# Kernel optimization log

Measured on AMD Instinct MI355X. Metric: run time of the kernel, lower is better.

Reference implementation:

```python
import jax, jax.numpy as jnp
import numpy as np


def setup_inputs() -> dict:
    key = jax.random.key(0)
    ks = jax.random.split(key, 7)
    B, D, d1, d2, d3 = 256, 256, 1024, 512, 256
    s = lambda f: 1.0 / np.sqrt(f)  # torch nn.Linear-style init scale
    return {
        "x": jax.random.normal(ks[0], (B, D), jnp.float32),
        "W1": jax.random.normal(ks[1], (d1, D), jnp.float32) * s(D),
        "b1": jax.random.normal(ks[2], (d1,), jnp.float32) * s(D),
        "W2": jax.random.normal(ks[3], (d2, d1), jnp.float32) * s(d1),
        "b2": jax.random.normal(ks[4], (d2,), jnp.float32) * s(d1),
        "W3": jax.random.normal(ks[5], (d3, d2), jnp.float32) * s(d2),
        "b3": jax.random.normal(ks[6], (d3,), jnp.float32) * s(d2),
        "k": 10,
    }


def _border_dists(x, W1, b1, W2, b2, W3, b3):
    # Layer 1: pre-activations and boundary distances. For the first layer the
    # effective linear map is W1 itself (shared across the batch).
    z1 = x @ W1.T + b1                                   # [B, d1]
    dist1 = jnp.abs(z1) / jnp.linalg.norm(W1, axis=1)    # [B, d1]
    m1 = (z1 > 0).astype(x.dtype)
    V1 = m1[:, :, None] * W1[None]                       # [B, d1, D] per-instance map after ReLU
    h1 = m1 * z1

    # Layer 2
    z2 = h1 @ W2.T + b2                                  # [B, d2]
    V2 = jnp.einsum('oi,bid->bod', W2, V1)               # [B, d2, D]
    dist2 = jnp.abs(z2) / jnp.linalg.norm(V2, axis=2)
    m2 = (z2 > 0).astype(x.dtype)
    h2 = m2 * z2

    # Layer 3
    z3 = h2 @ W3.T + b3                                  # [B, d3]
    V3 = jnp.einsum('oi,bid->bod', W3, m2[:, :, None] * V2)  # [B, d3, D]
    dist3 = jnp.abs(z3) / jnp.linalg.norm(V3, axis=2)

    return jnp.concatenate([dist1, dist2, dist3], axis=1)  # [B, d1+d2+d3]


def reference(x, W1, b1, W2, b2, W3, b3, k):
    dists = _border_dists(x, W1, b1, W2, b2, W3, b3)
    # smallest-k distances per instance via top_k on negated distances
    neg_top, _ = jax.lax.top_k(-dists, k)                # [B, k]
    return jnp.sum(-neg_top)                             # border-distance loss (scalar)
```

## Files before the change

kernel.cpp:

```cpp
#include <hip/hip_runtime.h>
#include <math.h>
#include <float.h>

#define B   256
#define D   256
#define D1  1024
#define D2  512
#define D3  256
#define NDIST (D1 + D2 + D3)
#define CQ  2.0f

typedef __attribute__((ext_vector_type(8))) short short8;
typedef __attribute__((ext_vector_type(4))) float f32x4;
typedef __attribute__((ext_vector_type(4))) int   i32x4;

__device__ __forceinline__ float waveReduceSum(float v) {
    #pragma unroll
    for (int off = 32; off > 0; off >>= 1)
        v += __shfl_down(v, off, 64);
    return v;
}
__device__ __forceinline__ float waveReduceMax(float v) {
    #pragma unroll
    for (int off = 32; off > 0; off >>= 1)
        v = fmaxf(v, __shfl_down(v, off, 64));
    return v;
}
__device__ __forceinline__ unsigned short f2bf(float f) {
    unsigned int u = __float_as_uint(f);
    u = (u + 0x7FFFu + ((u >> 16) & 1u)) >> 16;
    return (unsigned short)u;
}
__device__ __forceinline__ float bf2f(unsigned short h) {
    return __uint_as_float(((unsigned int)h) << 16);
}
__device__ __forceinline__ void gld16(const void* g, void* l) {
    __builtin_amdgcn_global_load_lds(
        (const __attribute__((address_space(1))) unsigned int*)g,
        (__attribute__((address_space(3))) unsigned int*)l, 16, 0, 0);
}
__device__ __forceinline__ int swz_src(int row, int lane) {
    return ((lane & 3) + ((row >> 1) & 3)) & 3;
}
__device__ __forceinline__ int swz_frag(int row, int quad) {
    return row * 32 + (((quad - ((row >> 1) & 3)) & 3) * 8);
}

__device__ __forceinline__ void split_job(const float* src, unsigned short* hi,
                                          unsigned short* lo, int off) {
    float4 v = *(const float4*)(src + off);
    ushort4 h, l;
    h.x = f2bf(v.x); l.x = f2bf(v.x - bf2f(h.x));
    h.y = f2bf(v.y); l.y = f2bf(v.y - bf2f(h.y));
    h.z = f2bf(v.z); l.z = f2bf(v.z - bf2f(h.z));
    h.w = f2bf(v.w); l.w = f2bf(v.w - bf2f(h.w));
    *(ushort4*)(hi + off) = h;
    *(ushort4*)(lo + off) = l;
}

__device__ __forceinline__ void split8(const float* p, short8& h8, short8& l8) {
    float4 a = *(const float4*)(p);
    float4 b = *(const float4*)(p + 4);
    float hv[8] = { a.x, a.y, a.z, a.w, b.x, b.y, b.z, b.w };
    #pragma unroll
    for (int q = 0; q < 8; q++) {
        unsigned short hh = f2bf(hv[q]);
        h8[q] = (short)hh;
        l8[q] = (short)f2bf(hv[q] - bf2f(hh));
    }
}

template <int KD, int KL>
__device__ __forceinline__ void mfma3_64(
    const unsigned short* __restrict__ Ahi, const unsigned short* __restrict__ Alo,
    const unsigned short* __restrict__ Bhi, const unsigned short* __restrict__ Blo,
    int m0, int n0, int k0, unsigned short* sm, f32x4 acc[2][2]) {
    int tid = threadIdx.x;
    int l = tid & 63, w = tid >> 6;
    int rsub = l >> 2;
    int quad = l >> 4, l16 = l & 15;
    int wm = (w >> 1) * 32, wn = (w & 1) * 32;
    unsigned short* sAh = sm;
    unsigned short* sAl = sm + 2048;
    unsigned short* sBh = sm + 4096;
    unsigned short* sBl = sm + 6144;
    ptrdiff_t dA = Alo - Ahi, dB = Blo - Bhi;
    int rloc = w * 16 + rsub;
    int c = swz_src(rloc, l);
    const unsigned short* pa = Ahi + (size_t)(m0 + rloc) * KD + k0 + c * 8;
    const unsigned short* pb = Bhi + (size_t)(n0 + rloc) * KD + k0 + c * 8;
    int aoff[2], boff[2];
    #pragma unroll
    for (int mt = 0; mt < 2; mt++) aoff[mt] = swz_frag(wm + mt * 16 + l16, quad);
    #pragma unroll
    for (int nt = 0; nt < 2; nt++) boff[nt] = swz_frag(wn + nt * 16 + l16, quad);
    for (int kk = 0; kk < KL; kk += 32) {
        gld16(pa + kk,      sAh + w * 512);
        gld16(pa + dA + kk, sAl + w * 512);
        gld16(pb + kk,      sBh + w * 512);
        gld16(pb + dB + kk, sBl + w * 512);
        __syncthreads();
        short8 ah[2], al[2], bh[2], bl[2];
        #pragma unroll
        for (int mt = 0; mt < 2; mt++) {
            ah[mt] = *(const short8*)(sAh + aoff[mt]);
            al[mt] = *(const short8*)(sAl + aoff[mt]);
        }
        #pragma unroll
        for (int nt = 0; nt < 2; nt++) {
            bh[nt] = *(const short8*)(sBh + boff[nt]);
            bl[nt] = *(const short8*)(sBl + boff[nt]);
        }
        #pragma unroll
        for (int mt = 0; mt < 2; mt++)
            #pragma unroll
            for (int nt = 0; nt < 2; nt++) {
                acc[mt][nt] = __builtin_amdgcn_mfma_f32_16x16x32_bf16(ah[mt], bh[nt], acc[mt][nt], 0, 0, 0);
                acc[mt][nt] = __builtin_amdgcn_mfma_f32_16x16x32_bf16(ah[mt], bl[nt], acc[mt][nt], 0, 0, 0);
                acc[mt][nt] = __builtin_amdgcn_mfma_f32_16x16x32_bf16(al[mt], bh[nt], acc[mt][nt], 0, 0, 0);
            }
        __syncthreads();
    }
}

__global__ __launch_bounds__(256) void k_l1p(
    const float* __restrict__ x, const float* __restrict__ W1,
    const float* __restrict__ W2, const float* __restrict__ W3,
    const float* __restrict__ b1,
    float* __restrict__ dists, unsigned char* __restrict__ m1q,
    unsigned short* __restrict__ h1hi, unsigned short* __restrict__ h1lo,
    float* __restrict__ zeros, float* __restrict__ outp,
    unsigned short* __restrict__ W2hi, unsigned short* __restrict__ W2lo,
    unsigned short* __restrict__ W3hi, unsigned short* __restrict__ W3lo,
    signed char* __restrict__ W1Ti8, float* __restrict__ saq,
    signed char* __restrict__ W2i8,  float* __restrict__ sbq,
    signed char* __restrict__ W3i8,  float* __restrict__ s3q,
    float* __restrict__ rn1) {
    __shared__ __align__(16) unsigned short sm[8192];
    int blk = blockIdx.x;
    int t = threadIdx.x;

    if (blk < 64) {
        unsigned short* sAh = sm;
        unsigned short* sAl = sm + 2048;
        unsigned short* sBh = sm + 4096;
        unsigned short* sBl = sm + 6144;
        int m0 = (blk & 3) * 64, n0 = (blk >> 2) * 64;
        int l = t & 63, w = t >> 6;
        int rsub = l >> 2;
        int quad = l >> 4, l16 = l & 15;
        int wm = (w >> 1) * 32, wn = (w & 1) * 32;
        int rloc = w * 16 + rsub;
        int c = swz_src(rloc, l);
        const float* pax = x + (size_t)(m0 + rloc) * D + c * 8;
        const float* pbw = W1 + (size_t)(n0 + rloc) * D + c * 8;
        int aoff[2], boff[2];
        #pragma unroll
        for (int mt = 0; mt < 2; mt++) aoff[mt] = swz_frag(wm + mt * 16 + l16, quad);
        #pragma unroll
        for (int nt = 0; nt < 2; nt++) boff[nt] = swz_frag(wn + nt * 16 + l16, quad);
        int wrA = w * 512 + l * 8;
        f32x4 acc[2][2] = {};
        for (int kk = 0; kk < D; kk += 32) {
            short8 ha, la, hb, lb;
            split8(pax + kk, ha, la);
            split8(pbw + kk, hb, lb);
            *(short8*)(sAh + wrA) = ha;
            *(short8*)(sAl + wrA) = la;
            *(short8*)(sBh + wrA) = hb;
            *(short8*)(sBl + wrA) = lb;
            __syncthreads();
            short8 ah[2], al[2], bh[2], bl[2];
            #pragma unroll
            for (int mt = 0; mt < 2; mt++) {
                ah[mt] = *(const short8*)(sAh + aoff[mt]);
                al[mt] = *(const short8*)(sAl + aoff[mt]);
            }
            #pragma unroll
            for (int nt = 0; nt < 2; nt++) {
                bh[nt] = *(const short8*)(sBh + boff[nt]);
                bl[nt] = *(const short8*)(sBl + boff[nt]);
            }
            #pragma unroll
            for (int mt = 0; mt < 2; mt++)
                #pragma unroll
                for (int nt = 0; nt < 2; nt++) {
                    acc[mt][nt] = __builtin_amdgcn_mfma_f32_16x16x32_bf16(ah[mt], bh[nt], acc[mt][nt], 0, 0, 0);
                    acc[mt][nt] = __builtin_amdgcn_mfma_f32_16x16x32_bf16(ah[mt], bl[nt], acc[mt][nt], 0, 0, 0);
                    acc[mt][nt] = __builtin_amdgcn_mfma_f32_16x16x32_bf16(al[mt], bh[nt], acc[mt][nt], 0, 0, 0);
                }
            __syncthreads();
        }
        #pragma unroll
        for (int mt = 0; mt < 2; mt++)
            #pragma unroll
            for (int nt = 0; nt < 2; nt++) {
                int n = n0 + wn + nt * 16 + l16;
                float bv = b1[n];
                #pragma unroll
                for (int r = 0; r < 4; r++) {
                    int m = m0 + wm + mt * 16 + quad * 4 + r;
                    float z = acc[mt][nt][r] + bv;
                    size_t idx = (size_t)m * D1 + n;
                    dists[idx] = fabsf(z);
                    m1q[idx] = (z > 0.f) ? 0xFFu : 0u;
                    float h = z > 0.f ? z : 0.f;
                    unsigned short hh = f2bf(h);
                    h1hi[idx] = hh;
                    h1lo[idx] = f2bf(h - bf2f(hh));
                }
            }
        return;
    }
    if (blk < 448) {
        if (blk == 64 && t == 0) outp[0] = 0.f;
        int i4 = (blk - 64) * 1024 + t * 4;
        *(float4*)(zeros + i4) = make_float4(0.f, 0.f, 0.f, 0.f);
        return;
    }
    if (blk < 960) {
        split_job(W2, W2hi, W2lo, (blk - 448) * 1024 + t * 4);
        return;
    }
    if (blk < 1088) {
        split_job(W3, W3hi, W3lo, (blk - 960) * 1024 + t * 4);
        return;
    }
    if (blk < 1120) {
        int ty = t >> 5, tx = t & 31;
        int d = (blk - 1088) * 8 + ty;
        float m = 0.f;
        for (int i = tx; i < D1; i += 32) m = fmaxf(m, fabsf(W1[(size_t)i * D + d]));
        #pragma unroll
        for (int off = 16; off > 0; off >>= 1) m = fmaxf(m, __shfl_down(m, off, 32));
        m = __shfl(m, 0, 32);
        m = fmaxf(m, 1e-20f);
        if (tx == 0) saq[d] = m / 127.f;
        float inv = 127.f / m;
        for (int i = tx; i < D1; i += 32) {
            int q = __float2int_rn(W1[(size_t)i * D + d] * inv);
            W1Ti8[(size_t)d * D1 + i] = (signed char)q;
        }
        return;
    }
    if (blk < 1248) {
        int o = (blk - 1120) * 4 + (t >> 6);
        int l = t & 63;
        const float* row = W2 + (size_t)o * D1;
        float m = 0.f;
        for (int tt = l; tt < D1; tt += 64) m = fmaxf(m, fabsf(row[tt]));
        m = waveReduceMax(m);
        m = __shfl(m, 0, 64);
        m = fmaxf(m, 1e-20f);
        if (l == 0) sbq[o] = m / 127.f;
        float inv = 127.f / m;
        for (int tt = l; tt < D1; tt += 64)
            W2i8[(size_t)o * D1 + tt] = (signed char)__float2int_rn(row[tt] * inv);
        return;
    }
    if (blk < 1312) {
        int p = (blk - 1248) * 4 + (t >> 6);
        int l = t & 63;
        const float* row = W3 + (size_t)p * D2;
        float m = 0.f;
        for (int tt = l; tt < D2; tt += 64) m = fmaxf(m, fabsf(row[tt]));
        m = waveReduceMax(m);
        m = __shfl(m, 0, 64);
        m = fmaxf(m, 1e-20f);
        if (l == 0) s3q[p] = m / 127.f;
        float inv = 127.f / m;
        for (int tt = l; tt < D2; tt += 64)
            W3i8[(size_t)p * D2 + tt] = (signed char)__float2int_rn(row[tt] * inv);
        return;
    }
    {
        int gw = (blk - 1312) * 4 + (t >> 6);
        int lane = t & 63;
        const float* row = W1 + (size_t)gw * D;
        float s = 0.f;
        for (int tt = lane; tt < D; tt += 64) { float v = row[tt]; s += v * v; }
        s = waveReduceSum(s);
        if (lane == 0) rn1[gw] = sqrtf(s);
    }
}

__global__ __launch_bounds__(256) void k_big1(
    const unsigned short* __restrict__ h1hi, const unsigned short* __restrict__ h1lo,
    const unsigned short* __restrict__ W2hi, const unsigned short* __restrict__ W2lo,
    float* __restrict__ z2,
    const signed char* __restrict__ W1Ti8,
    const signed char* __restrict__ W2i8,
    const unsigned char* __restrict__ m1q,
    const float* __restrict__ saq,
    const float* __restrict__ sbq,
    signed char* __restrict__ qV2,
    float* __restrict__ norm2) {
    __shared__ __align__(16) unsigned char smem[65536];
    int bid = blockIdx.x;

    if (bid < 128) {
        unsigned short* sm = (unsigned short*)smem;
        int m0 = (bid & 3) * 64, n0 = ((bid >> 2) & 7) * 64, k0 = (bid >> 5) * 256;
        f32x4 acc[2][2] = {};
        mfma3_64<D1, 256>(h1hi, h1lo, W2hi, W2lo, m0, n0, k0, sm, acc);
        int l = threadIdx.x & 63, w = threadIdx.x >> 6;
        int quad = l >> 4, l16 = l & 15;
        int wm = (w >> 1) * 32, wn = (w & 1) * 32;
        #pragma unroll
        for (int mt = 0; mt < 2; mt++)
            #pragma unroll
            for (int nt = 0; nt < 2; nt++) {
                int n = n0 + wn + nt * 16 + l16;
                #pragma unroll
                for (int r = 0; r < 4; r++) {
                    int m = m0 + wm + mt * 16 + quad * 4 + r;
                    atomicAdd(&z2[(size_t)m * D2 + n], acc[mt][nt][r]);
                }
            }
        return;
    }

    int j = bid - 128;
    int m0 = (j & 1) * 128;
    int o0 = ((j >> 1) & 3) * 128;
    int b = j >> 3;
    int tid = threadIdx.x;
    int l = tid & 63, w = tid >> 6;
    int quad = l >> 4, l16 = l & 15;
    int wm = (w >> 1) * 64, wn = (w & 1) * 64;
    const unsigned char* mrow = m1q + (size_t)b * D1;

    const signed char* pa[4];
    const signed char* pb[4];
    int lrow = l >> 3, ls = l & 7;
    #pragma unroll
    for (int r = 0; r < 4; r++) {
        int row = r * 32 + w * 8 + lrow;
        int c = (ls + (row & 7)) & 7;
        pa[r] = W1Ti8 + (size_t)(m0 + row) * D1 + c * 16;
        pb[r] = W2i8 + (size_t)(o0 + row) * D1 + c * 16;
    }
    int aoff[4][2], boff[4][2];
    #pragma unroll
    for (int mt = 0; mt < 4; mt++) {
        int tr = wm + mt * 16 + l16;
        #pragma unroll
        for (int ks = 0; ks < 2; ks++)
            aoff[mt][ks] = tr * 128 + (((ks * 4 + quad) - (tr & 7)) & 7) * 16;
    }
    #pragma unroll
    for (int nt = 0; nt < 4; nt++) {
        int tr = wn + nt * 16 + l16;
        #pragma unroll
        for (int ks = 0; ks < 2; ks++)
            boff[nt][ks] = tr * 128 + (((ks * 4 + quad) - (tr & 7)) & 7) * 16;
    }

    i32x4 acc[4][4];
    #pragma unroll
    for (int i = 0; i < 4; i++)
        #pragma unroll
        for (int jj = 0; jj < 4; jj++) acc[i][jj] = (i32x4)0;

    {
        signed char* buf0 = (signed char*)smem;
        #pragma unroll
        for (int r = 0; r < 4; r++) {
            gld16(pa[r], buf0 + r * 4096 + w * 1024);
            gld16(pb[r], buf0 + 16384 + r * 4096 + w * 1024);
        }
    }
    i32x4 mv0 = *(const i32x4*)(mrow + quad * 16);
    i32x4 mv1 = *(const i32x4*)(mrow + 64 + quad * 16);
    __syncthreads();

    #pragma unroll
    for (int t = 0; t < 8; t++) {
        signed char* bufc = (signed char*)smem + ((t & 1) << 15);
        signed char* bufn = (signed char*)smem + (((t + 1) & 1) << 15);
        i32x4 nmv0 = mv0, nmv1 = mv1;
        if (t < 7) {
            int kn = (t + 1) * 128;
            #pragma unroll
            for (int r = 0; r < 4; r++) {
                gld16(pa[r] + kn, bufn + r * 4096 + w * 1024);
                gld16(pb[r] + kn, bufn + 16384 + r * 4096 + w * 1024);
            }
            nmv0 = *(const i32x4*)(mrow + kn + quad * 16);
            nmv1 = *(const i32x4*)(mrow + kn + 64 + quad * 16);
        }
        const signed char* As = bufc;
        const signed char* Bs = bufc + 16384;
        #pragma unroll
        for (int ks = 0; ks < 2; ks++) {
            i32x4 mv = ks ? mv1 : mv0;
            i32x4 a[4], bq[4];
            #pragma unroll
            for (int mt = 0; mt < 4; mt++)
                a[mt] = (*(const i32x4*)(As + aoff[mt][ks])) & mv;
            #pragma unroll
            for (int nt = 0; nt < 4; nt++)
                bq[nt] = *(const i32x4*)(Bs + boff[nt][ks]);
            #pragma unroll
            for (int mt = 0; mt < 4; mt++)
                #pragma unroll
                for (int nt = 0; nt < 4; nt++)
                    acc[mt][nt] = __builtin_amdgcn_mfma_i32_16x16x64_i8(
                        a[mt], bq[nt], acc[mt][nt], 0, 0, 0);
        }
        __syncthreads();
        mv0 = nmv0; mv1 = nmv1;
    }

    float sad[4][4];
    #pragma unroll
    for (int mt = 0; mt < 4; mt++)
        #pragma unroll
        for (int r = 0; r < 4; r++)
            sad[mt][r] = saq[m0 + wm + mt * 16 + quad * 4 + r];
    float sbv[4], sbdq[4];
    #pragma unroll
    for (int nt = 0; nt < 4; nt++) {
        sbv[nt] = sbq[o0 + wn + nt * 16 + l16];
        sbdq[nt] = sbv[nt] * (1.0f / CQ);
    }

    float nrm[4] = {0.f, 0.f, 0.f, 0.f};
    signed char* qb = qV2 + (size_t)b * (D * D2);
    #pragma unroll
    for (int mt = 0; mt < 4; mt++) {
        int dbase = m0 + wm + mt * 16 + quad * 4;
        #pragma unroll
        for (int r = 0; r < 4; r++) {
            float sa = sad[mt][r];
            size_t rowoff = (size_t)(dbase + r) * D2;
            #pragma unroll
            for (int nt = 0; nt < 4; nt++) {
                float tv = (float)acc[mt][nt][r];
                float u = tv * sa;
                nrm[nt] = fmaf(u, u, nrm[nt]);
                int qi = __float2int_rn(tv * sbdq[nt]);
                qi = max(-127, min(127, qi));
                qb[rowoff + o0 + wn + nt * 16 + l16] = (signed char)qi;
            }
        }
    }
    #pragma unroll
    for (int nt = 0; nt < 4; nt++) {
        float s = nrm[nt] * (sbv[nt] * sbv[nt]);
        s += __shfl_down(s, 32, 64);
        s += __shfl_down(s, 16, 64);
        if (l < 16)
            atomicAdd(&norm2[(size_t)b * D2 + o0 + wn + nt * 16 + l], s);
    }
}

__global__ __launch_bounds__(256) void k_big2(
    const float* __restrict__ z2,
    const float* __restrict__ b2,
    const unsigned short* __restrict__ W3hi, const unsigned short* __restrict__ W3lo,
    float* __restrict__ z3,
    const signed char* __restrict__ W3i8,
    const signed char* __restrict__ qV2,
    const float* __restrict__ saq,
    const float* __restrict__ s3q,
    float* __restrict__ norm3) {
    __shared__ __align__(16) unsigned char smem[66048];
    int bid = blockIdx.x;
    int tid = threadIdx.x;

    if (bid < 32) {
        unsigned short* sAh = (unsigned short*)smem;
        unsigned short* sAl = sAh + 2048;
        unsigned short* sBh = sAh + 4096;
        unsigned short* sBl = sAh + 6144;
        int m0 = (bid & 3) * 64, n0 = ((bid >> 2) & 3) * 64, k0 = (bid >> 4) * 256;
        int l = tid & 63, w = tid >> 6;
        int rsub = l >> 2;
        int quad = l >> 4, l16 = l & 15;
        int wm = (w >> 1) * 32, wn = (w & 1) * 32;
        int rloc = w * 16 + rsub;
        int c = swz_src(rloc, l);
        const float* pz  = z2 + (size_t)(m0 + rloc) * D2 + k0 + c * 8;
        const float* pbi = b2 + k0 + c * 8;
        const unsigned short* pb = W3hi + (size_t)(n0 + rloc) * D2 + k0 + c * 8;
        ptrdiff_t dB = W3lo - W3hi;
        int aoff[2], boff[2];
        #pragma unroll
        for (int mt = 0; mt < 2; mt++) aoff[mt] = swz_frag(wm + mt * 16 + l16, quad);
        #pragma unroll
        for (int nt = 0; nt < 2; nt++) boff[nt] = swz_frag(wn + nt * 16 + l16, quad);
        int wrA = w * 512 + l * 8;
        f32x4 acc[2][2] = {};
        for (int kk = 0; kk < 256; kk += 32) {
            gld16(pb + kk,      sBh + w * 512);
            gld16(pb + dB + kk, sBl + w * 512);
            float4 za = *(const float4*)(pz + kk);
            float4 zb = *(const float4*)(pz + kk + 4);
            float4 ba = *(const float4*)(pbi + kk);
            float4 bb = *(const float4*)(pbi + kk + 4);
            float hv[8] = { za.x + ba.x, za.y + ba.y, za.z + ba.z, za.w + ba.w,
                            zb.x + bb.x, zb.y + bb.y, zb.z + bb.z, zb.w + bb.w };
            short8 h8, l8;
            #pragma unroll
            for (int q2 = 0; q2 < 8; q2++) {
                float h = hv[q2] > 0.f ? hv[q2] : 0.f;
                unsigned short hh = f2bf(h);
                h8[q2] = (short)hh;
                l8[q2] = (short)f2bf(h - bf2f(hh));
            }
            *(short8*)(sAh + wrA) = h8;
            *(short8*)(sAl + wrA) = l8;
            __syncthreads();
            short8 ah[2], al[2], bh[2], bl[2];
            #pragma unroll
            for (int mt = 0; mt < 2; mt++) {
                ah[mt] = *(const short8*)(sAh + aoff[mt]);
                al[mt] = *(const short8*)(sAl + aoff[mt]);
            }
            #pragma unroll
            for (int nt = 0; nt < 2; nt++) {
                bh[nt] = *(const short8*)(sBh + boff[nt]);
                bl[nt] = *(const short8*)(sBl + boff[nt]);
            }
            #pragma unroll
            for (int mt = 0; mt < 2; mt++)
                #pragma unroll
                for (int nt = 0; nt < 2; nt++) {
                    acc[mt][nt] = __builtin_amdgcn_mfma_f32_16x16x32_bf16(ah[mt], bh[nt], acc[mt][nt], 0, 0, 0);
                    acc[mt][nt] = __builtin_amdgcn_mfma_f32_16x16x32_bf16(ah[mt], bl[nt], acc[mt][nt], 0, 0, 0);
                    acc[mt][nt] = __builtin_amdgcn_mfma_f32_16x16x32_bf16(al[mt], bh[nt], acc[mt][nt], 0, 0, 0);
                }
            __syncthreads();
        }
        #pragma unroll
        for (int mt = 0; mt < 2; mt++)
            #pragma unroll
            for (int nt = 0; nt < 2; nt++) {
                int n = n0 + wn + nt * 16 + l16;
                #pragma unroll
                for (int r = 0; r < 4; r++) {
                    int m = m0 + wm + mt * 16 + quad * 4 + r;
                    atomicAdd(&z3[(size_t)m * D3 + n], acc[mt][nt][r]);
                }
            }
        return;
    }

    int j = bid - 32;
    unsigned char* mbuf = (unsigned char*)smem + 65536;
    int m0 = (j & 1) * 128;
    int n0 = ((j >> 1) & 1) * 128;
    int bc = j >> 2;
    int l = tid & 63, w = tid >> 6;
    int quad = l >> 4, l16 = l & 15;
    int wm = (w >> 1) * 64, wn = (w & 1) * 64;
    const signed char* Bsrc = qV2 + (size_t)bc * (D * D2);

    {
        #pragma unroll
        for (int rr = 0; rr < 2; rr++) {
            int o = tid * 2 + rr;
            float z = z2[(size_t)bc * D2 + o] + b2[o];
            mbuf[o] = (z > 0.f) ? 0xFFu : 0u;
        }
    }

    const signed char* pa[4];
    const signed char* pb[4];
    int lrow = l >> 3, ls = l & 7;
    #pragma unroll
    for (int r = 0; r < 4; r++) {
        int row = r * 32 + w * 8 + lrow;
        int c = (ls + (row & 7)) & 7;
        pa[r] = W3i8 + (size_t)(m0 + row) * D2 + c * 16;
        pb[r] = Bsrc + (size_t)(n0 + row) * D2 + c * 16;
    }
    int aoff[4][2], boff[4][2];
    #pragma unroll
    for (int mt = 0; mt < 4; mt++) {
        int tr = wm + mt * 16 + l16;
        #pragma unroll
        for (int ks = 0; ks < 2; ks++)
            aoff[mt][ks] = tr * 128 + (((ks * 4 + quad) - (tr & 7)) & 7) * 16;
    }
    #pragma unroll
    for (int nt = 0; nt < 4; nt++) {
        int tr = wn + nt * 16 + l16;
        #pragma unroll
        for (int ks = 0; ks < 2; ks++)
            boff[nt][ks] = tr * 128 + (((ks * 4 + quad) - (tr & 7)) & 7) * 16;
    }

    i32x4 acc[4][4];
    #pragma unroll
    for (int i = 0; i < 4; i++)
        #pragma unroll
        for (int jj = 0; jj < 4; jj++) acc[i][jj] = (i32x4)0;

    {
        signed char* buf0 = (signed char*)smem;
        #pragma unroll
        for (int r = 0; r < 4; r++) {
            gld16(pa[r], buf0 + r * 4096 + w * 1024);
            gld16(pb[r], buf0 + 16384 + r * 4096 + w * 1024);
        }
    }
    __syncthreads();

    #pragma unroll
    for (int t = 0; t < 4; t++) {
        signed char* bufc = (signed char*)smem + ((t & 1) << 15);
        signed char* bufn = (signed char*)smem + (((t + 1) & 1) << 15);
        if (t < 3) {
            int kn = (t + 1) * 128;
            #pragma unroll
            for (int r = 0; r < 4; r++) {
                gld16(pa[r] + kn, bufn + r * 4096 + w * 1024);
                gld16(pb[r] + kn, bufn + 16384 + r * 4096 + w * 1024);
            }
        }
        int kk = t * 128;
        i32x4 mv0 = *(const i32x4*)(mbuf + kk + quad * 16);
        i32x4 mv1 = *(const i32x4*)(mbuf + kk + 64 + quad * 16);
        const signed char* As = bufc;
        const signed char* Bs = bufc + 16384;
        #pragma unroll
        for (int ks = 0; ks < 2; ks++) {
            i32x4 mv = ks ? mv1 : mv0;
            i32x4 a[4], bq[4];
            #pragma unroll
            for (int mt = 0; mt < 4; mt++)
                a[mt] = *(const i32x4*)(As + aoff[mt][ks]);
            #pragma unroll
            for (int nt = 0; nt < 4; nt++)
                bq[nt] = (*(const i32x4*)(Bs + boff[nt][ks])) & mv;
            #pragma unroll
            for (int mt = 0; mt < 4; mt++)
                #pragma unroll
                for (int nt = 0; nt < 4; nt++)
                    acc[mt][nt] = __builtin_amdgcn_mfma_i32_16x16x64_i8(
                        a[mt], bq[nt], acc[mt][nt], 0, 0, 0);
        }
        __syncthreads();
    }

    float saCQ[4];
    #pragma unroll
    for (int nt = 0; nt < 4; nt++)
        saCQ[nt] = saq[n0 + wn + nt * 16 + l16] * CQ;

    #pragma unroll
    for (int mt = 0; mt < 4; mt++)
        #pragma unroll
        for (int r = 0; r < 4; r++) {
            float s = 0.f;
            #pragma unroll
            for (int nt = 0; nt < 4; nt++) {
                float v = (float)acc[mt][nt][r] * saCQ[nt];
                s += v * v;
            }
            s += __shfl_down(s, 8, 64);
            s += __shfl_down(s, 4, 64);
            s += __shfl_down(s, 2, 64);
            s += __shfl_down(s, 1, 64);
            if (l16 == 0) {
                int p = m0 + wm + mt * 16 + quad * 4 + r;
                float s3 = s3q[p];
                atomicAdd(&norm3[(size_t)bc * D3 + p], s * s3 * s3);
            }
        }
}

__global__ __launch_bounds__(256) void k_topk(
    const float* __restrict__ dists,
    const float* __restrict__ rn1,
    const float* __restrict__ z2, const float* __restrict__ b2,
    const float* __restrict__ norm2,
    const float* __restrict__ z3, const float* __restrict__ b3,
    const float* __restrict__ norm3,
    const int* __restrict__ kp, float* __restrict__ outp) {
    int t = threadIdx.x;
    int wv = t >> 6, lane = t & 63;
    int b = blockIdx.x * 4 + wv;
    float lv[28];
    #pragma unroll
    for (int j = 0; j < 16; j++) {
        int n = lane + 64 * j;
        lv[j] = dists[(size_t)b * D1 + n] / rn1[n];
    }
    #pragma unroll
    for (int j = 16; j < 24; j++) {
        int o = lane + 64 * (j - 16);
        float zz = z2[(size_t)b * D2 + o] + b2[o];
        lv[j] = fabsf(zz) / sqrtf(norm2[(size_t)b * D2 + o]);
    }
    #pragma unroll
    for (int j = 24; j < 28; j++) {
        int p = lane + 64 * (j - 24);
        float zz = z3[(size_t)b * D3 + p] + b3[p];
        lv[j] = fabsf(zz) / sqrtf(norm3[(size_t)b * D3 + p]);
    }
    int k = *kp;
    if (k > NDIST) k = NDIST;
    float sum = 0.f;
    for (int it = 0; it < k; it++) {
        float mv = lv[0]; int mj = 0;
        #pragma unroll
        for (int j = 1; j < 28; j++)
            if (lv[j] < mv) { mv = lv[j]; mj = j; }
        unsigned long long key =
            ((unsigned long long)__float_as_uint(mv) << 32) | (unsigned)(lane * 32 + mj);
        #pragma unroll
        for (int off = 1; off < 64; off <<= 1) {
            unsigned long long o = __shfl_xor(key, off, 64);
            if (o < key) key = o;
        }
        sum += __uint_as_float((unsigned)(key >> 32));
        int wl = (int)((key >> 5) & 63u), wj = (int)(key & 31u);
        if (lane == wl) lv[wj] = FLT_MAX;
    }
    if (lane == 0) atomicAdd(outp, sum);
}

extern "C" void kernel_launch(void* const* d_in, const int* in_sizes, int n_in,
                              void* d_out, int out_size, void* d_ws, size_t ws_size,
                              hipStream_t stream) {
    const float* x  = (const float*)d_in[0];
    const float* W1 = (const float*)d_in[1];
    const float* b1 = (const float*)d_in[2];
    const float* W2 = (const float*)d_in[3];
    const float* b2 = (const float*)d_in[4];
    const float* W3 = (const float*)d_in[5];
    const float* b3 = (const float*)d_in[6];
    const int*   kp = (const int*)d_in[7];
    float* outp = (float*)d_out;

    float* fp = (float*)d_ws;
    float* rn1     = fp;                          fp += D1;
    float* dists   = fp;                          fp += (size_t)B * D1;
    float* saq     = fp;                          fp += D;
    float* sbq     = fp;                          fp += D2;
    float* s3q     = fp;                          fp += D3;
    float* z2      = fp;                          fp += (size_t)B * D2;
    float* z3      = fp;                          fp += (size_t)B * D3;
    float* norm2   = fp;                          fp += (size_t)B * D2;
    float* norm3   = fp;                          fp += (size_t)B * D3;
    unsigned short* up = (unsigned short*)fp;
    unsigned short* W2hi  = up;  up += (size_t)D2 * D1;
    unsigned short* W2lo  = up;  up += (size_t)D2 * D1;
    unsigned short* W3hi  = up;  up += (size_t)D3 * D2;
    unsigned short* W3lo  = up;  up += (size_t)D3 * D2;
    unsigned short* h1hi  = up;  up += (size_t)B * D1;
    unsigned short* h1lo  = up;  up += (size_t)B * D1;
    signed char*    cp = (signed char*)up;
    signed char*    W1Ti8 = cp;  cp += (size_t)D * D1;
    signed char*    W2i8  = cp;  cp += (size_t)D2 * D1;
    signed char*    W3i8  = cp;  cp += (size_t)D3 * D2;
    unsigned char*  m1q   = (unsigned char*)cp;  cp += (size_t)B * D1;
    signed char*    qV2   = cp;

    k_l1p<<<1568, 256, 0, stream>>>(x, W1, W2, W3, b1,
                                    dists, m1q, h1hi, h1lo,
                                    z2, outp, W2hi, W2lo, W3hi, W3lo,
                                    W1Ti8, saq, W2i8, sbq, W3i8, s3q, rn1);

    k_big1<<<2176, 256, 0, stream>>>(h1hi, h1lo, W2hi, W2lo, z2,
                                     W1Ti8, W2i8, m1q, saq, sbq, qV2, norm2);

    k_big2<<<1056, 256, 0, stream>>>(z2, b2, W3hi, W3lo, z3,
                                     W3i8, qV2, saq, s3q, norm3);

    k_topk<<<B / 4, 256, 0, stream>>>(dists, rn1, z2, b2, norm2, z3, b3, norm3,
                                      kp, outp);
}
```

Baseline: 175.4 us.

## Process two batch rows per k_big1 block and single-buffer k_big2 tiles

k_big1 now computes two batch instances per block, reusing each loaded W1T/W2 tile for two sets of masked MFMAs. That halves the global loads of the weight tiles and the block count, at the cost of double the accumulator registers. Launch bounds now request 2 blocks per CU, and the mask rows are staged in shared memory. k_big2 drops its double buffering in favour of a single 32KB tile buffer so more blocks fit per CU, which gives up load/compute overlap inside a block.

Result: faster. 160.9 us (-8.3%).

```diff
diff --git a/kernel.cpp b/kernel.cpp
--- a/kernel.cpp
+++ b/kernel.cpp
@@ -284,7 +284,7 @@
     }
 }
 
-__global__ __launch_bounds__(256) void k_big1(
+__global__ __launch_bounds__(256, 2) void k_big1(
     const unsigned short* __restrict__ h1hi, const unsigned short* __restrict__ h1lo,
     const unsigned short* __restrict__ W2hi, const unsigned short* __restrict__ W2lo,
     float* __restrict__ z2,
@@ -295,7 +295,7 @@
     const float* __restrict__ sbq,
     signed char* __restrict__ qV2,
     float* __restrict__ norm2) {
-    __shared__ __align__(16) unsigned char smem[65536];
+    __shared__ __align__(16) unsigned char smem[67584];
     int bid = blockIdx.x;
 
     if (bid < 128) {
@@ -323,12 +323,14 @@
     int j = bid - 128;
     int m0 = (j & 1) * 128;
     int o0 = ((j >> 1) & 3) * 128;
-    int b = j >> 3;
+    int b0 = (j >> 3) * 2;
     int tid = threadIdx.x;
     int l = tid & 63, w = tid >> 6;
     int quad = l >> 4, l16 = l & 15;
     int wm = (w >> 1) * 64, wn = (w & 1) * 64;
-    const unsigned char* mrow = m1q + (size_t)b * D1;
+    unsigned char* mbuf = (unsigned char*)smem + 65536;
+
+    *(int2*)(mbuf + tid * 8) = *(const int2*)(m1q + (size_t)b0 * D1 + tid * 8);
 
     const signed char* pa[4];
     const signed char* pb[4];
@@ -356,11 +358,13 @@
             boff[nt][ks] = tr * 128 + (((ks * 4 + quad) - (tr & 7)) & 7) * 16;
     }
 
-    i32x4 acc[4][4];
-    #pragma unroll
-    for (int i = 0; i < 4; i++)
-        #pragma unroll
-        for (int jj = 0; jj < 4; jj++) acc[i][jj] = (i32x4)0;
+    i32x4 acc[2][4][4];
+    #pragma unroll
+    for (int g = 0; g < 2; g++)
+        #pragma unroll
+        for (int i = 0; i < 4; i++)
+            #pragma unroll
+            for (int jj = 0; jj < 4; jj++) acc[g][i][jj] = (i32x4)0;
 
     {
         signed char* buf0 = (signed char*)smem;
@@ -370,15 +374,12 @@
             gld16(pb[r], buf0 + 16384 + r * 4096 + w * 1024);
         }
     }
-    i32x4 mv0 = *(const i32x4*)(mrow + quad * 16);
-    i32x4 mv1 = *(const i32x4*)(mrow + 64 + quad * 16);
     __syncthreads();
 
     #pragma unroll
     for (int t = 0; t < 8; t++) {
         signed char* bufc = (signed char*)smem + ((t & 1) << 15);
         signed char* bufn = (signed char*)smem + (((t + 1) & 1) << 15);
-        i32x4 nmv0 = mv0, nmv1 = mv1;
         if (t < 7) {
             int kn = (t + 1) * 128;
             #pragma unroll
@@ -386,30 +387,35 @@
                 gld16(pa[r] + kn, bufn + r * 4096 + w * 1024);
                 gld16(pb[r] + kn, bufn + 16384 + r * 4096 + w * 1024);
             }
-            nmv0 = *(const i32x4*)(mrow + kn + quad * 16);
-            nmv1 = *(const i32x4*)(mrow + kn + 64 + quad * 16);
         }
         const signed char* As = bufc;
         const signed char* Bs = bufc + 16384;
         #pragma unroll
         for (int ks = 0; ks < 2; ks++) {
-            i32x4 mv = ks ? mv1 : mv0;
+            i32x4 mva = *(const i32x4*)(mbuf +        t * 128 + ks * 64 + quad * 16);
+            i32x4 mvb = *(const i32x4*)(mbuf + 1024 + t * 128 + ks * 64 + quad * 16);
             i32x4 a[4], bq[4];
             #pragma unroll
             for (int mt = 0; mt < 4; mt++)
-                a[mt] = (*(const i32x4*)(As + aoff[mt][ks])) & mv;
+                a[mt] = *(const i32x4*)(As + aoff[mt][ks]);
             #pragma unroll
             for (int nt = 0; nt < 4; nt++)
                 bq[nt] = *(const i32x4*)(Bs + boff[nt][ks]);
             #pragma unroll
-            for (int mt = 0; mt < 4; mt++)
+            for (int mt = 0; mt < 4; mt++) {
+                i32x4 a0 = a[mt] & mva;
+                i32x4 a1 = a[mt] & mvb;
                 #pragma unroll
                 for (int nt = 0; nt < 4; nt++)
-                    acc[mt][nt] = __builtin_amdgcn_mfma_i32_16x16x64_i8(
-                        a[mt], bq[nt], acc[mt][nt], 0, 0, 0);
+                    acc[0][mt][nt] = __builtin_amdgcn_mfma_i32_16x16x64_i8(
+                        a0, bq[nt], acc[0][mt][nt], 0, 0, 0);
+                #pragma unroll
+                for (int nt = 0; nt < 4; nt++)
+                    acc[1][mt][nt] = __builtin_amdgcn_mfma_i32_16x16x64_i8(
+                        a1, bq[nt], acc[1][mt][nt], 0, 0, 0);
+            }
         }
         __syncthreads();
-        mv0 = nmv0; mv1 = nmv1;
     }
 
     float sad[4][4];
@@ -425,33 +431,37 @@
         sbdq[nt] = sbv[nt] * (1.0f / CQ);
     }
 
-    float nrm[4] = {0.f, 0.f, 0.f, 0.f};
-    signed char* qb = qV2 + (size_t)b * (D * D2);
-    #pragma unroll
-    for (int mt = 0; mt < 4; mt++) {
-        int dbase = m0 + wm + mt * 16 + quad * 4;
-        #pragma unroll
-        for (int r = 0; r < 4; r++) {
-            float sa = sad[mt][r];
-            size_t rowoff = (size_t)(dbase + r) * D2;
-            #pragma unroll
-            for (int nt = 0; nt < 4; nt++) {
-                float tv = (float)acc[mt][nt][r];
-                float u = tv * sa;
-                nrm[nt] = fmaf(u, u, nrm[nt]);
-                int qi = __float2int_rn(tv * sbdq[nt]);
-                qi = max(-127, min(127, qi));
-                qb[rowoff + o0 + wn + nt * 16 + l16] = (signed char)qi;
-            }
-        }
-    }
-    #pragma unroll
-    for (int nt = 0; nt < 4; nt++) {
-        float s = nrm[nt] * (sbv[nt] * sbv[nt]);
-        s += __shfl_down(s, 32, 64);
-        s += __shfl_down(s, 16, 64);
-        if (l < 16)
-            atomicAdd(&norm2[(size_t)b * D2 + o0 + wn + nt * 16 + l], s);
+    #pragma unroll
+    for (int g = 0; g < 2; g++) {
+        int bg = b0 + g;
+        float nrm[4] = {0.f, 0.f, 0.f, 0.f};
+        signed char* qb = qV2 + (size_t)bg * (D * D2);
+        #pragma unroll
+        for (int mt = 0; mt < 4; mt++) {
+            int dbase = m0 + wm + mt * 16 + quad * 4;
+            #pragma unroll
+            for (int r = 0; r < 4; r++) {
+                float sa = sad[mt][r];
+                size_t rowoff = (size_t)(dbase + r) * D2;
+                #pragma unroll
+                for (int nt = 0; nt < 4; nt++) {
+                    float tv = (float)acc[g][mt][nt][r];
+                    float u = tv * sa;
+                    nrm[nt] = fmaf(u, u, nrm[nt]);
+                    int qi = __float2int_rn(tv * sbdq[nt]);
+                    qi = max(-127, min(127, qi));
+                    qb[rowoff + o0 + wn + nt * 16 + l16] = (signed char)qi;
+                }
+            }
+        }
+        #pragma unroll
+        for (int nt = 0; nt < 4; nt++) {
+            float s = nrm[nt] * (sbv[nt] * sbv[nt]);
+            s += __shfl_down(s, 32, 64);
+            s += __shfl_down(s, 16, 64);
+            if (l < 16)
+                atomicAdd(&norm2[(size_t)bg * D2 + o0 + wn + nt * 16 + l], s);
+        }
     }
 }
 
@@ -465,7 +475,7 @@
     const float* __restrict__ saq,
     const float* __restrict__ s3q,
     float* __restrict__ norm3) {
-    __shared__ __align__(16) unsigned char smem[66048];
+    __shared__ __align__(16) unsigned char smem[33280];
     int bid = blockIdx.x;
     int tid = threadIdx.x;
 
@@ -548,7 +558,9 @@
     }
 
     int j = bid - 32;
-    unsigned char* mbuf = (unsigned char*)smem + 65536;
+    signed char* As = (signed char*)smem;
+    signed char* Bs = (signed char*)smem + 16384;
+    unsigned char* mbuf = (unsigned char*)smem + 32768;
     int m0 = (j & 1) * 128;
     int n0 = ((j >> 1) & 1) * 128;
     int bc = j >> 2;
@@ -565,6 +577,7 @@
             mbuf[o] = (z > 0.f) ? 0xFFu : 0u;
         }
     }
+    __syncthreads();
 
     const signed char* pa[4];
     const signed char* pb[4];
@@ -598,33 +611,15 @@
         #pragma unroll
         for (int jj = 0; jj < 4; jj++) acc[i][jj] = (i32x4)0;
 
-    {
-        signed char* buf0 = (signed char*)smem;
+    for (int kk = 0; kk < D2; kk += 128) {
         #pragma unroll
         for (int r = 0; r < 4; r++) {
-            gld16(pa[r], buf0 + r * 4096 + w * 1024);
-            gld16(pb[r], buf0 + 16384 + r * 4096 + w * 1024);
-        }
-    }
-    __syncthreads();
-
-    #pragma unroll
-    for (int t = 0; t < 4; t++) {
-        signed char* bufc = (signed char*)smem + ((t & 1) << 15);
-        signed char* bufn = (signed char*)smem + (((t + 1) & 1) << 15);
-        if (t < 3) {
-            int kn = (t + 1) * 128;
-            #pragma unroll
-            for (int r = 0; r < 4; r++) {
-                gld16(pa[r] + kn, bufn + r * 4096 + w * 1024);
-                gld16(pb[r] + kn, bufn + 16384 + r * 4096 + w * 1024);
-            }
-        }
-        int kk = t * 128;
+            gld16(pa[r] + kk, As + r * 4096 + w * 1024);
+            gld16(pb[r] + kk, Bs + r * 4096 + w * 1024);
+        }
+        __syncthreads();
         i32x4 mv0 = *(const i32x4*)(mbuf + kk + quad * 16);
         i32x4 mv1 = *(const i32x4*)(mbuf + kk + 64 + quad * 16);
-        const signed char* As = bufc;
-        const signed char* Bs = bufc + 16384;
         #pragma unroll
         for (int ks = 0; ks < 2; ks++) {
             i32x4 mv = ks ? mv1 : mv0;
@@ -765,7 +760,7 @@
                                     z2, outp, W2hi, W2lo, W3hi, W3lo,
                                     W1Ti8, saq, W2i8, sbq, W3i8, s3q, rn1);
 
-    k_big1<<<2176, 256, 0, stream>>>(h1hi, h1lo, W2hi, W2lo, z2,
+    k_big1<<<1152, 256, 0, stream>>>(h1hi, h1lo, W2hi, W2lo, z2,
                                      W1Ti8, W2i8, m1q, saq, sbq, qV2, norm2);
 
     k_big2<<<1056, 256, 0, stream>>>(z2, b2, W3hi, W3lo, z3,
```
